# Optimization experiments

Hardware: AMD Instinct MI355X
Metric: run time of the kernel (lower is better)

Reference implementation:

```python
import jax, jax.numpy as jnp
import numpy as np

K = 16  # num_neighbors
L = 3   # stacked PointTransformer layers


def _mlp2(x, w1, b1, w2, b2):
    return jax.nn.relu(x @ w1 + b1) @ w2 + b2


def setup_inputs() -> dict:
    key = jax.random.key(0)
    ks = jax.random.split(key, 10)
    B, N, D = 2, 8192, 3
    HP, HA = 32, 12  # pos_mlp hidden, attn_mlp hidden (3*4)
    f = lambda k, shp, s: jax.random.normal(k, shp, dtype=jnp.float32) * s
    return {
        "feats": f(ks[0], (B, N, D), 1.0),
        "pos": f(ks[1], (B, N, 3), 1.0),
        "mask": jnp.ones((B, N), dtype=bool),  # unused by PT.forward
        "w_qkv": f(ks[2], (L, D, 3 * D), 1.0 / np.sqrt(D)),
        "pos_w1": f(ks[3], (L, 3, HP), 1.0 / np.sqrt(3.0)),
        "pos_b1": jnp.zeros((L, HP), jnp.float32),
        "pos_w2": f(ks[4], (L, HP, D), 1.0 / np.sqrt(HP)),
        "pos_b2": jnp.zeros((L, D), jnp.float32),
        "attn_w1": f(ks[5], (L, D, HA), 1.0 / np.sqrt(D)),
        "attn_b1": jnp.zeros((L, HA), jnp.float32),
        "attn_w2": f(ks[6], (L, HA, D), 1.0 / np.sqrt(HA)),
        "attn_b2": jnp.zeros((L, D), jnp.float32),
        "lin_w": f(ks[7], (D, 2), 1.0 / np.sqrt(D)),
        "lin_b": jnp.zeros((2,), jnp.float32),
    }


def reference(feats, pos, mask, w_qkv, pos_w1, pos_b1, pos_w2, pos_b2,
              attn_w1, attn_b1, attn_w2, attn_b2, lin_w, lin_b):
    # kNN indices from pairwise squared distances (monotonic in the norm the
    # original uses, so topk-smallest gives identical neighbor sets).
    sq = jnp.sum(pos * pos, axis=-1)                               # [B,N]
    d2 = sq[:, :, None] + sq[:, None, :] - 2.0 * jnp.einsum('bic,bjc->bij', pos, pos)
    _, idx = jax.lax.top_k(-d2, K)                                 # [B,N,K]

    gather = jax.vmap(lambda t, i: t[i])                           # [B,N,d],[B,N,K]->[B,N,K,d]
    pos_j = gather(pos, idx)                                       # [B,N,K,3]
    rel_pos = pos[:, :, None, :] - pos_j                           # [B,N,K,3]

    h = feats
    for l in range(L):
        qkv = h @ w_qkv[l]                                         # [B,N,9]
        q, k, v = jnp.split(qkv, 3, axis=-1)
        k_j = gather(k, idx)                                       # [B,N,K,3]
        v_j = gather(v, idx)
        rel_emb = _mlp2(rel_pos, pos_w1[l], pos_b1[l], pos_w2[l], pos_b2[l])
        qk_rel = q[:, :, None, :] - k_j
        sim = _mlp2(qk_rel + rel_emb, attn_w1[l], attn_b1[l], attn_w2[l], attn_b2[l])
        attn = jax.nn.softmax(sim, axis=-2)                        # softmax over neighbors
        agg = jnp.einsum('bijd,bijd->bid', attn, v_j + rel_emb)    # [B,N,3]
        h = jax.nn.sigmoid(agg)
    out = h @ lin_w + lin_b                                        # [B,N,2]
    return jax.nn.softmax(out, axis=2)
```

## Files before the change

kernel.cpp:

```cpp
#include <hip/hip_runtime.h>
#include <math.h>

#define N_PTS 8192
#define BATCH 2
#define KNB 16
#define NQ (BATCH * N_PTS)

#define H    0.35f
#define INVH (1.0f / 0.35f)
#define NC   30
#define LBOX (0.5f * H * NC)
#define NCELL (NC * NC * NC)
#define MCELL (2 * NCELL)
#define NROW1 9
#define NROWT 43
#define SLOWG 1024
#define FINF 3.4e38f

typedef unsigned long long u64;

__device__ __forceinline__ float med3f(float a, float b, float c) {
#if __has_builtin(__builtin_amdgcn_fmed3f)
    return __builtin_amdgcn_fmed3f(a, b, c);
#else
    return fmaxf(fminf(a, b), fminf(fmaxf(a, b), c));
#endif
}

__device__ __forceinline__ unsigned sortable(float x) {
    unsigned u = __float_as_uint(x);
    return u ^ ((unsigned)((int)u >> 31) | 0x80000000u);
}

__device__ __forceinline__ void ins_u64(u64 (&pk)[KNB], u64 key) {
    if (key < pk[0]) {
#pragma unroll
        for (int s = 0; s < KNB; ++s) {
            const u64 ds1 = (s < KNB - 1) ? pk[s + 1] : 0ull;
            const bool c0 = key < pk[s];
            const bool c1 = key < ds1;
            pk[s] = c1 ? ds1 : (c0 ? key : pk[s]);
        }
    }
}

__device__ __forceinline__ void merge64_u64(u64 (&pk)[KNB]) {
#pragma unroll
    for (int mm = 1; mm <= 32; mm <<= 1) {
        u64 L[KNB];
#pragma unroll
        for (int i = 0; i < KNB; ++i) {
            const u64 a = pk[i];
            const u64 c = __shfl_xor(pk[KNB - 1 - i], mm);
            L[i] = a < c ? a : c;
        }
#pragma unroll
        for (int dd = 8; dd >= 1; dd >>= 1) {
#pragma unroll
            for (int i = 0; i < KNB; ++i) {
                if ((i & dd) == 0) {
                    const u64 hi = L[i] > L[i | dd] ? L[i] : L[i | dd];
                    const u64 lo = L[i] > L[i | dd] ? L[i | dd] : L[i];
                    L[i] = hi; L[i | dd] = lo;
                }
            }
        }
#pragma unroll
        for (int i = 0; i < KNB; ++i) pk[i] = L[i];
    }
}

__device__ __forceinline__ void merge64_f(float (&d)[KNB]) {
#pragma unroll
    for (int mm = 1; mm <= 32; mm <<= 1) {
        float L[KNB];
#pragma unroll
        for (int i = 0; i < KNB; ++i)
            L[i] = fminf(d[i], __shfl_xor(d[KNB - 1 - i], mm));
#pragma unroll
        for (int dd = 8; dd >= 1; dd >>= 1) {
#pragma unroll
            for (int i = 0; i < KNB; ++i) {
                if ((i & dd) == 0) {
                    const float hi = fmaxf(L[i], L[i | dd]);
                    const float lo = fminf(L[i], L[i | dd]);
                    L[i] = hi; L[i | dd] = lo;
                }
            }
        }
#pragma unroll
        for (int i = 0; i < KNB; ++i) d[i] = L[i];
    }
}

__global__ __launch_bounds__(256) void kcount(const float* __restrict__ pos,
                                              int* __restrict__ cnt,
                                              int* __restrict__ cellid) {
    const int g = blockIdx.x * 256 + threadIdx.x;
    const int b = g >> 13;
    const float x = pos[g * 3 + 0], y = pos[g * 3 + 1], z = pos[g * 3 + 2];
    int cx = (int)floorf((x + LBOX) * INVH); cx = min(max(cx, 0), NC - 1);
    int cy = (int)floorf((y + LBOX) * INVH); cy = min(max(cy, 0), NC - 1);
    int cz = (int)floorf((z + LBOX) * INVH); cz = min(max(cz, 0), NC - 1);
    const int c = (((b * NC) + cz) * NC + cy) * NC + cx;
    cellid[g] = c;
    atomicAdd(&cnt[c], 1);
}

__global__ __launch_bounds__(1024) void kscan1(const int* __restrict__ cnt,
                                               int* __restrict__ scanned,
                                               int* __restrict__ bsum) {
    __shared__ int sh[1024];
    const int t = threadIdx.x;
    const int idx = blockIdx.x * 1024 + t;
    int v = (idx < MCELL) ? cnt[idx] : 0;
    sh[t] = v;
    __syncthreads();
    for (int off = 1; off < 1024; off <<= 1) {
        const int add = (t >= off) ? sh[t - off] : 0;
        __syncthreads();
        sh[t] += add;
        __syncthreads();
    }
    if (idx < MCELL) scanned[idx] = sh[t];
    if (t == 1023) bsum[blockIdx.x] = sh[1023];
}

__global__ __launch_bounds__(1024) void kscan2(const int* __restrict__ scanned,
                                               const int* __restrict__ bsum,
                                               int* __restrict__ cell_start) {
    __shared__ int soff;
    const int t = threadIdx.x;
    const int blk = blockIdx.x;
    const int idx = blk * 1024 + t;
    if (t == 0) {
        int s = 0;
        for (int k = 0; k < blk; ++k) s += bsum[k];
        soff = s;
    }
    __syncthreads();
    if (idx < MCELL) cell_start[idx + 1] = scanned[idx] + soff;
    if (idx == 0) cell_start[0] = 0;
}

__global__ __launch_bounds__(256) void kscatter(const float* __restrict__ pos,
                                                const int* __restrict__ cellid,
                                                const int* __restrict__ cell_start,
                                                int* __restrict__ cnt2,
                                                float4* __restrict__ spp,
                                                int* __restrict__ sidx) {
    const int g = blockIdx.x * 256 + threadIdx.x;
    const int c = cellid[g];
    const int off = atomicAdd(&cnt2[c], 1);
    const int p = cell_start[c] + off;
    const float x = pos[g * 3 + 0], y = pos[g * 3 + 1], z = pos[g * 3 + 2];
    spp[p] = make_float4(-2.f * x, -2.f * y, -2.f * z, fmaf(x, x, fmaf(y, y, z * z)));
    sidx[p] = g & (N_PTS - 1);
}

__global__ __launch_bounds__(64, 4) void ksearch_fast(const float4* __restrict__ spp,
                                                      const int* __restrict__ sidx,
                                                      const int* __restrict__ cs,
                                                      int* __restrict__ knn,
                                                      int* __restrict__ ovf_list,
                                                      int* __restrict__ ovf_cnt) {
    __shared__ int rstL[4][NROWT];
    __shared__ int psL[4][NROWT + 1];
    const int tid = threadIdx.x;
    const int li  = tid & 15;
    const int gq  = tid >> 4;
    const int sq  = blockIdx.x * 4 + gq;
    const int b   = sq >> 13;

    {
        __shared__ int cntL[4][NROWT];
        for (int t = tid; t < 4 * NROWT; t += 64) {
            const int q = t / NROWT, r = t % NROWT;
            const int sq2 = blockIdx.x * 4 + q;
            const int b2  = sq2 >> 13;
            const float4 m2 = spp[sq2];
            const float px = -0.5f * m2.x, py = -0.5f * m2.y, pz = -0.5f * m2.z;
            int c2x = (int)floorf((px + LBOX) * INVH); c2x = min(max(c2x, 0), NC - 1);
            int c2y = (int)floorf((py + LBOX) * INVH); c2y = min(max(c2y, 0), NC - 1);
            int c2z = (int)floorf((pz + LBOX) * INVH); c2z = min(max(c2z, 0), NC - 1);

            int st = 0, en = 0;
            int z, y, xlo, xhi;
            bool ok = true;
            if (r < NROW1) {
                z = c2z + r / 3 - 1;
                y = c2y + (r % 3) - 1;
                xlo = max(c2x - 1, 0); xhi = min(c2x + 1, NC - 1);
            } else {
                const int rr = r - NROW1;
                if (rr < 10) {
                    z = c2z + (rr < 5 ? -2 : 2);
                    y = c2y + (rr % 5) - 2;
                    xlo = max(c2x - 2, 0); xhi = min(c2x + 2, NC - 1);
                } else if (rr < 16) {
                    const int k = rr - 10;
                    z = c2z + (k % 3) - 1;
                    y = c2y + (k < 3 ? -2 : 2);
                    xlo = max(c2x - 2, 0); xhi = min(c2x + 2, NC - 1);
                } else {
                    const int k = rr - 16;
                    const int m = k % 9;
                    z = c2z + m / 3 - 1;
                    y = c2y + (m % 3) - 1;
                    const int xx = c2x + (k < 9 ? -2 : 2);
                    xlo = xhi = xx;
                    ok = (xx >= 0) && (xx < NC);
                }
            }
            if (ok && z >= 0 && z < NC && y >= 0 && y < NC) {
                const int rowb = (((b2 * NC) + z) * NC + y) * NC;
                st = cs[rowb + xlo];
                en = cs[rowb + xhi + 1];
            }
            rstL[q][r] = st; cntL[q][r] = en - st;
        }
        __syncthreads();
        if (tid < 4) {
            int acc = 0;
            psL[tid][0] = 0;
            for (int r = 0; r < NROWT; ++r) { acc += cntL[tid][r]; psL[tid][r + 1] = acc; }
        }
        __syncthreads();
    }

    const float4 me = spp[sq];
    const float qx = -0.5f * me.x, qy = -0.5f * me.y, qz = -0.5f * me.z;
    const float qsq = me.w;
    int cx = (int)floorf((qx + LBOX) * INVH); cx = min(max(cx, 0), NC - 1);
    int cy = (int)floorf((qy + LBOX) * INVH); cy = min(max(cy, 0), NC - 1);
    int cz = (int)floorf((qz + LBOX) * INVH); cz = min(max(cz, 0), NC - 1);

    const int tot1 = psL[gq][NROW1];
    const int tot2 = psL[gq][NROWT];

    float d[KNB];
#pragma unroll
    for (int k = 0; k < KNB; ++k) d[k] = FINF;

    int row = 0;
    int t = li;

    auto scan1_flat = [&](int limit) {
        while (t < limit) {
            int pp[8]; bool vv[8];
#pragma unroll
            for (int u = 0; u < 8; ++u) {
                const int tt = t + u * 16;
                vv[u] = (tt < limit);
                int p = sq;
                if (vv[u]) {
                    while (tt >= psL[gq][row + 1]) ++row;
                    p = rstL[gq][row] + (tt - psL[gq][row]);
                }
                pp[u] = p;
            }
            float4 v[8];
#pragma unroll
            for (int u = 0; u < 8; ++u) v[u] = spp[pp[u]];
#pragma unroll
            for (int u = 0; u < 8; ++u) {
                const float x = vv[u] ? fmaf(qx, v[u].x, fmaf(qy, v[u].y, fmaf(qz, v[u].z, v[u].w)))
                                      : FINF;
                if (x < d[0]) {
#pragma unroll
                    for (int s = 0; s < KNB - 1; ++s) d[s] = med3f(d[s], d[s + 1], x);
                    d[KNB - 1] = fminf(d[KNB - 1], x);
                }
            }
            t += 128;
        }
    };

    auto boundtest = [&](int R) -> bool {
        const float bxl = fmaf((float)(cx - R), H, -LBOX);
        const float bxh = fmaf((float)(cx + R + 1), H, -LBOX);
        const float byl = fmaf((float)(cy - R), H, -LBOX);
        const float byh = fmaf((float)(cy + R + 1), H, -LBOX);
        const float bzl = fmaf((float)(cz - R), H, -LBOX);
        const float bzh = fmaf((float)(cz + R + 1), H, -LBOX);
        const float m = fminf(fminf(fminf(qx - bxl, bxh - qx),
                                    fminf(qy - byl, byh - qy)),
                              fminf(qz - bzl, bzh - qz));
        if (!(m > 0.f)) return false;
        const float Bf = fmaf(m, m, -1e-4f) - qsq;
        int c = 0;
#pragma unroll
        for (int k = 0; k < KNB; ++k) c += (d[k] <= Bf) ? 1 : 0;
#pragma unroll
        for (int off = 1; off < 16; off <<= 1) c += __shfl_xor(c, off);
        return c >= KNB;
    };

    scan1_flat(tot1);
    const bool done1 = boundtest(1);
    bool ovf = false;
    if (!done1) {
        scan1_flat(tot2);
        if (!boundtest(2)) ovf = true;
    }
    if (ovf) {
        if (li == 0) { const int s2 = atomicAdd(ovf_cnt, 1); ovf_list[s2] = sq; }
        return;
    }
    const int tot = done1 ? tot1 : tot2;

#pragma unroll
    for (int mm = 1; mm <= 8; mm <<= 1) {
        float L[KNB];
#pragma unroll
        for (int i = 0; i < KNB; ++i)
            L[i] = fminf(d[i], __shfl_xor(d[KNB - 1 - i], mm));
#pragma unroll
        for (int dd = 8; dd >= 1; dd >>= 1) {
#pragma unroll
            for (int i = 0; i < KNB; ++i) {
                if ((i & dd) == 0) {
                    const float hi = fmaxf(L[i], L[i | dd]);
                    const float lo = fminf(L[i], L[i | dd]);
                    L[i] = hi; L[i | dd] = lo;
                }
            }
        }
#pragma unroll
        for (int i = 0; i < KNB; ++i) d[i] = L[i];
    }
    const float thr = d[0];

    u64 pk[KNB];
#pragma unroll
    for (int k = 0; k < KNB; ++k) pk[k] = 0xFFFFFFFFFFFFFFFFull;

    row = 0;
    int t2 = li;
    while (t2 < tot) {
        int pp[8]; bool vv[8];
#pragma unroll
        for (int u = 0; u < 8; ++u) {
            const int tt = t2 + u * 16;
            vv[u] = (tt < tot);
            int p = sq;
            if (vv[u]) {
                while (tt >= psL[gq][row + 1]) ++row;
                p = rstL[gq][row] + (tt - psL[gq][row]);
            }
            pp[u] = p;
        }
        float4 v[8];
#pragma unroll
        for (int u = 0; u < 8; ++u) v[u] = spp[pp[u]];
#pragma unroll
        for (int u = 0; u < 8; ++u) {
            const float x = vv[u] ? fmaf(qx, v[u].x, fmaf(qy, v[u].y, fmaf(qz, v[u].z, v[u].w)))
                                  : FINF;
            if (x <= thr) {
                ins_u64(pk, ((u64)sortable(x) << 32) | (unsigned)sidx[pp[u]]);
            }
        }
        t2 += 128;
    }

#pragma unroll
    for (int mm = 1; mm <= 8; mm <<= 1) {
        u64 L[KNB];
#pragma unroll
        for (int i = 0; i < KNB; ++i) {
            const u64 a = pk[i];
            const u64 c = __shfl_xor(pk[KNB - 1 - i], mm);
            L[i] = a < c ? a : c;
        }
#pragma unroll
        for (int dd = 8; dd >= 1; dd >>= 1) {
#pragma unroll
            for (int i = 0; i < KNB; ++i) {
                if ((i & dd) == 0) {
                    const u64 hi = L[i] > L[i | dd] ? L[i] : L[i | dd];
                    const u64 lo = L[i] > L[i | dd] ? L[i | dd] : L[i];
                    L[i] = hi; L[i | dd] = lo;
                }
            }
        }
#pragma unroll
        for (int i = 0; i < KNB; ++i) pk[i] = L[i];
    }

    const int qorig = sidx[sq];
    const int obase = ((b << 13) + qorig) * KNB;
    u64 sel = pk[0];
#pragma unroll
    for (int s = 1; s < KNB; ++s) sel = (li == s) ? pk[s] : sel;
    knn[obase + li] = (int)(unsigned)(sel & 0xFFFFFFFFull);
}

__global__ __launch_bounds__(64, 4) void kslow(const float4* __restrict__ spp,
                                               const int* __restrict__ sidx,
                                               int* __restrict__ knn,
                                               const int* __restrict__ ovf_list,
                                               const int* __restrict__ ovf_cnt) {
    const int lane = threadIdx.x;
    const int nov = *ovf_cnt;

    for (int w = blockIdx.x; w < nov; w += SLOWG) {
        const int sq = ovf_list[w];
        const int b  = sq >> 13;
        const float4 me = spp[sq];
        const float qx = -0.5f * me.x, qy = -0.5f * me.y, qz = -0.5f * me.z;
        const int base = b << 13;

        float d[KNB];
#pragma unroll
        for (int k = 0; k < KNB; ++k) d[k] = FINF;

        for (int t0 = 0; t0 < 16; ++t0) {
            const int tb = base + lane + t0 * 512;
            float4 v[8];
#pragma unroll
            for (int u = 0; u < 8; ++u) v[u] = spp[tb + u * 64];
#pragma unroll
            for (int u = 0; u < 8; ++u) {
                const float x = fmaf(qx, v[u].x, fmaf(qy, v[u].y, fmaf(qz, v[u].z, v[u].w)));
                if (x < d[0]) {
#pragma unroll
                    for (int s = 0; s < KNB - 1; ++s) d[s] = med3f(d[s], d[s + 1], x);
                    d[KNB - 1] = fminf(d[KNB - 1], x);
                }
            }
        }
        merge64_f(d);
        const float thr = d[0];

        u64 pk[KNB];
#pragma unroll
        for (int k = 0; k < KNB; ++k) pk[k] = 0xFFFFFFFFFFFFFFFFull;

        for (int t0 = 0; t0 < 16; ++t0) {
            const int tb = base + lane + t0 * 512;
            float4 v[8];
#pragma unroll
            for (int u = 0; u < 8; ++u) v[u] = spp[tb + u * 64];
#pragma unroll
            for (int u = 0; u < 8; ++u) {
                const float x = fmaf(qx, v[u].x, fmaf(qy, v[u].y, fmaf(qz, v[u].z, v[u].w)));
                if (x <= thr) {
                    ins_u64(pk, ((u64)sortable(x) << 32) | (unsigned)sidx[tb + u * 64]);
                }
            }
        }
        merge64_u64(pk);

        const int qorig = sidx[sq];
        const int obase = ((b << 13) + qorig) * KNB;
        u64 sel = pk[0];
#pragma unroll
        for (int s = 1; s < KNB; ++s) sel = (lane == s) ? pk[s] : sel;
        if (lane < KNB) knn[obase + lane] = (int)(unsigned)(sel & 0xFFFFFFFFull);
    }
}

__global__ __launch_bounds__(256) void pt_layer_f(const float* __restrict__ hin,
                                                  const float* __restrict__ pos,
                                                  const int* __restrict__ knn,
                                                  const float* __restrict__ wqkv,
                                                  const float* __restrict__ pw1,
                                                  const float* __restrict__ pb1,
                                                  const float* __restrict__ pw2,
                                                  const float* __restrict__ pb2,
                                                  const float* __restrict__ aw1,
                                                  const float* __restrict__ ab1,
                                                  const float* __restrict__ aw2,
                                                  const float* __restrict__ ab2,
                                                  float* __restrict__ hout,
                                                  const float* __restrict__ lw,
                                                  const float* __restrict__ lb,
                                                  float* __restrict__ out,
                                                  int last) {
    const int gt = blockIdx.x * 256 + threadIdx.x;
    const int qg = gt >> 4;
    const int j  = gt & 15;
    const int b  = qg >> 13;
    const int jj = knn[qg * KNB + j] & (N_PTS - 1);
    const int g  = (b << 13) + jj;

    const float hi0 = hin[qg * 3 + 0], hi1 = hin[qg * 3 + 1], hi2 = hin[qg * 3 + 2];
    const float hj0 = hin[g * 3 + 0],  hj1 = hin[g * 3 + 1],  hj2 = hin[g * 3 + 2];
    const float rx = pos[qg * 3 + 0] - pos[g * 3 + 0];
    const float ry = pos[qg * 3 + 1] - pos[g * 3 + 1];
    const float rz = pos[qg * 3 + 2] - pos[g * 3 + 2];

    const float q0 = fmaf(hi0, wqkv[0], fmaf(hi1, wqkv[9],  hi2 * wqkv[18]));
    const float q1 = fmaf(hi0, wqkv[1], fmaf(hi1, wqkv[10], hi2 * wqkv[19]));
    const float q2 = fmaf(hi0, wqkv[2], fmaf(hi1, wqkv[11], hi2 * wqkv[20]));
    const float k0 = fmaf(hj0, wqkv[3], fmaf(hj1, wqkv[12], hj2 * wqkv[21]));
    const float k1 = fmaf(hj0, wqkv[4], fmaf(hj1, wqkv[13], hj2 * wqkv[22]));
    const float k2 = fmaf(hj0, wqkv[5], fmaf(hj1, wqkv[14], hj2 * wqkv[23]));
    const float v0 = fmaf(hj0, wqkv[6], fmaf(hj1, wqkv[15], hj2 * wqkv[24]));
    const float v1 = fmaf(hj0, wqkv[7], fmaf(hj1, wqkv[16], hj2 * wqkv[25]));
    const float v2 = fmaf(hj0, wqkv[8], fmaf(hj1, wqkv[17], hj2 * wqkv[26]));

    float e0 = pb2[0], e1 = pb2[1], e2 = pb2[2];
#pragma unroll
    for (int hh = 0; hh < 32; ++hh) {
        float t = fmaf(rx, pw1[hh], fmaf(ry, pw1[32 + hh], fmaf(rz, pw1[64 + hh], pb1[hh])));
        t = fmaxf(t, 0.0f);
        e0 = fmaf(t, pw2[hh * 3 + 0], e0);
        e1 = fmaf(t, pw2[hh * 3 + 1], e1);
        e2 = fmaf(t, pw2[hh * 3 + 2], e2);
    }

    const float x0 = q0 - k0 + e0;
    const float x1 = q1 - k1 + e1;
    const float x2 = q2 - k2 + e2;

    float s0 = ab2[0], s1 = ab2[1], s2 = ab2[2];
#pragma unroll
    for (int hh = 0; hh < 12; ++hh) {
        float t = fmaf(x0, aw1[hh], fmaf(x1, aw1[12 + hh], fmaf(x2, aw1[24 + hh], ab1[hh])));
        t = fmaxf(t, 0.0f);
        s0 = fmaf(t, aw2[hh * 3 + 0], s0);
        s1 = fmaf(t, aw2[hh * 3 + 1], s1);
        s2 = fmaf(t, aw2[hh * 3 + 2], s2);
    }

    const float w0 = v0 + e0, w1 = v1 + e1, w2 = v2 + e2;

    float m0 = s0, m1 = s1, m2 = s2;
#pragma unroll
    for (int off = 1; off < 16; off <<= 1) {
        m0 = fmaxf(m0, __shfl_xor(m0, off));
        m1 = fmaxf(m1, __shfl_xor(m1, off));
        m2 = fmaxf(m2, __shfl_xor(m2, off));
    }
    const float ex0 = __expf(s0 - m0), ex1 = __expf(s1 - m1), ex2 = __expf(s2 - m2);
    float n0 = ex0 * w0, n1 = ex1 * w1, n2 = ex2 * w2;
    float den0 = ex0, den1 = ex1, den2 = ex2;
#pragma unroll
    for (int off = 1; off < 16; off <<= 1) {
        den0 += __shfl_xor(den0, off); n0 += __shfl_xor(n0, off);
        den1 += __shfl_xor(den1, off); n1 += __shfl_xor(n1, off);
        den2 += __shfl_xor(den2, off); n2 += __shfl_xor(n2, off);
    }

    if (j == 0) {
        const float h0 = 1.f / (1.f + __expf(-(n0 / den0)));
        const float h1 = 1.f / (1.f + __expf(-(n1 / den1)));
        const float h2 = 1.f / (1.f + __expf(-(n2 / den2)));
        if (!last) {
            hout[qg * 3 + 0] = h0;
            hout[qg * 3 + 1] = h1;
            hout[qg * 3 + 2] = h2;
        } else {
            const float o0 = fmaf(h0, lw[0], fmaf(h1, lw[2], fmaf(h2, lw[4], lb[0])));
            const float o1 = fmaf(h0, lw[1], fmaf(h1, lw[3], fmaf(h2, lw[5], lb[1])));
            const float mm = fmaxf(o0, o1);
            const float ea = __expf(o0 - mm), eb = __expf(o1 - mm);
            const float inv = 1.f / (ea + eb);
            out[qg * 2 + 0] = ea * inv;
            out[qg * 2 + 1] = eb * inv;
        }
    }
}

extern "C" void kernel_launch(void* const* d_in, const int* in_sizes, int n_in,
                              void* d_out, int out_size, void* d_ws, size_t ws_size,
                              hipStream_t stream) {
    const float* feats = (const float*)d_in[0];
    const float* pos   = (const float*)d_in[1];
    const float* wqkv = (const float*)d_in[3];
    const float* pw1  = (const float*)d_in[4];
    const float* pb1  = (const float*)d_in[5];
    const float* pw2  = (const float*)d_in[6];
    const float* pb2  = (const float*)d_in[7];
    const float* aw1  = (const float*)d_in[8];
    const float* ab1  = (const float*)d_in[9];
    const float* aw2  = (const float*)d_in[10];
    const float* ab2  = (const float*)d_in[11];
    const float* lw   = (const float*)d_in[12];
    const float* lb   = (const float*)d_in[13];
    float* out = (float*)d_out;

    size_t o = 0;
    auto take = [&](size_t bytes) { size_t r = o; o += (bytes + 15) & ~(size_t)15; return r; };
    const size_t o_cnt   = take((size_t)(2 * MCELL + 4) * 4);
    const size_t o_scan  = take((size_t)MCELL * 4);
    const size_t o_cs    = take((size_t)(MCELL + 1) * 4);
    const size_t o_bsum  = take((size_t)256 * 4);
    const size_t o_cid   = take((size_t)NQ * 4);
    const size_t o_spp   = take((size_t)NQ * 16);
    const size_t o_sidx  = take((size_t)NQ * 4);
    const size_t o_knn   = take((size_t)NQ * KNB * 4);
    const size_t o_ovfl  = take((size_t)NQ * 4);
    const size_t o_hA    = take((size_t)NQ * 3 * 4);
    const size_t o_hB    = take((size_t)NQ * 3 * 4);
    if (ws_size < o) return;

    char* ws = (char*)d_ws;
    int*    cnt     = (int*)(ws + o_cnt);
    int*    cnt2    = cnt + MCELL;
    int*    ovf_cnt = cnt + 2 * MCELL;
    int*    scan  = (int*)(ws + o_scan);
    int*    cs    = (int*)(ws + o_cs);
    int*    bsum  = (int*)(ws + o_bsum);
    int*    cid   = (int*)(ws + o_cid);
    float4* spp   = (float4*)(ws + o_spp);
    int*    sidx  = (int*)(ws + o_sidx);
    int*    knn   = (int*)(ws + o_knn);
    int*    ovfl  = (int*)(ws + o_ovfl);
    float*  hA    = (float*)(ws + o_hA);
    float*  hB    = (float*)(ws + o_hB);

    const int nscan = (MCELL + 1023) / 1024;

    hipMemsetAsync(cnt, 0, (size_t)(2 * MCELL + 1) * 4, stream);
    kcount<<<NQ / 256, 256, 0, stream>>>(pos, cnt, cid);
    kscan1<<<nscan, 1024, 0, stream>>>(cnt, scan, bsum);
    kscan2<<<nscan, 1024, 0, stream>>>(scan, bsum, cs);
    kscatter<<<NQ / 256, 256, 0, stream>>>(pos, cid, cs, cnt2, spp, sidx);
    ksearch_fast<<<NQ / 4, 64, 0, stream>>>(spp, sidx, cs, knn, ovfl, ovf_cnt);
    kslow<<<SLOWG, 64, 0, stream>>>(spp, sidx, knn, ovfl, ovf_cnt);

    pt_layer_f<<<NQ * 16 / 256, 256, 0, stream>>>(feats, pos, knn,
        wqkv + 0, pw1 + 0, pb1 + 0, pw2 + 0, pb2 + 0,
        aw1 + 0, ab1 + 0, aw2 + 0, ab2 + 0,
        hA, lw, lb, out, 0);
    pt_layer_f<<<NQ * 16 / 256, 256, 0, stream>>>(hA, pos, knn,
        wqkv + 27, pw1 + 96, pb1 + 32, pw2 + 96, pb2 + 3,
        aw1 + 36, ab1 + 12, aw2 + 36, ab2 + 3,
        hB, lw, lb, out, 0);
    pt_layer_f<<<NQ * 16 / 256, 256, 0, stream>>>(hB, pos, knn,
        wqkv + 54, pw1 + 192, pb1 + 64, pw2 + 192, pb2 + 6,
        aw1 + 72, ab1 + 24, aw2 + 72, ab2 + 6,
        hB, lw, lb, out, 1);
}
```

Baseline: 126.6 us.

## Split brute-force overflow kNN search across four wavefronts per query

The fallback brute-force kNN kernel now uses four wavefronts per overflow query instead of one. Each wave scans a quarter of the batch's points, and the partial top-16 lists are merged through shared memory, both for the distance threshold and for the final packed index list. This cuts the serial scan length per query and adds block-level syncs plus an extra merge step. It also lowers the occupancy bound per block. The gain depends on how many queries overflow, which may be few.

```diff
diff --git a/kernel.cpp b/kernel.cpp
--- a/kernel.cpp
+++ b/kernel.cpp
@@ -396,12 +396,16 @@
     knn[obase + li] = (int)(unsigned)(sel & 0xFFFFFFFFull);
 }
 
-__global__ __launch_bounds__(64, 4) void kslow(const float4* __restrict__ spp,
-                                               const int* __restrict__ sidx,
-                                               int* __restrict__ knn,
-                                               const int* __restrict__ ovf_list,
-                                               const int* __restrict__ ovf_cnt) {
-    const int lane = threadIdx.x;
+__global__ __launch_bounds__(256, 2) void kslow(const float4* __restrict__ spp,
+                                                const int* __restrict__ sidx,
+                                                int* __restrict__ knn,
+                                                const int* __restrict__ ovf_list,
+                                                const int* __restrict__ ovf_cnt) {
+    __shared__ float shf[4][KNB];
+    __shared__ u64  shp[4][KNB];
+    const int tid  = threadIdx.x;
+    const int wv   = tid >> 6;
+    const int lane = tid & 63;
     const int nov = *ovf_cnt;
 
     for (int w = blockIdx.x; w < nov; w += SLOWG) {
@@ -409,14 +413,15 @@
         const int b  = sq >> 13;
         const float4 me = spp[sq];
         const float qx = -0.5f * me.x, qy = -0.5f * me.y, qz = -0.5f * me.z;
-        const int base = b << 13;
+        const int qbase = (b << 13) + wv * 2048;
 
         float d[KNB];
 #pragma unroll
         for (int k = 0; k < KNB; ++k) d[k] = FINF;
 
-        for (int t0 = 0; t0 < 16; ++t0) {
-            const int tb = base + lane + t0 * 512;
+#pragma unroll
+        for (int t0 = 0; t0 < 4; ++t0) {
+            const int tb = qbase + lane + t0 * 512;
             float4 v[8];
 #pragma unroll
             for (int u = 0; u < 8; ++u) v[u] = spp[tb + u * 64];
@@ -431,14 +436,23 @@
             }
         }
         merge64_f(d);
-        const float thr = d[0];
+        if (lane < KNB) shf[wv][lane] = d[lane];
+        __syncthreads();
+
+        float dm[KNB];
+#pragma unroll
+        for (int i = 0; i < KNB - 1; ++i) dm[i] = FINF;
+        dm[KNB - 1] = shf[lane >> 4][lane & 15];
+        merge64_f(dm);
+        const float thr = dm[0];
 
         u64 pk[KNB];
 #pragma unroll
         for (int k = 0; k < KNB; ++k) pk[k] = 0xFFFFFFFFFFFFFFFFull;
 
-        for (int t0 = 0; t0 < 16; ++t0) {
-            const int tb = base + lane + t0 * 512;
+#pragma unroll
+        for (int t0 = 0; t0 < 4; ++t0) {
+            const int tb = qbase + lane + t0 * 512;
             float4 v[8];
 #pragma unroll
             for (int u = 0; u < 8; ++u) v[u] = spp[tb + u * 64];
@@ -451,13 +465,24 @@
             }
         }
         merge64_u64(pk);
-
-        const int qorig = sidx[sq];
-        const int obase = ((b << 13) + qorig) * KNB;
-        u64 sel = pk[0];
-#pragma unroll
-        for (int s = 1; s < KNB; ++s) sel = (lane == s) ? pk[s] : sel;
-        if (lane < KNB) knn[obase + lane] = (int)(unsigned)(sel & 0xFFFFFFFFull);
+        if (lane < KNB) shp[wv][lane] = pk[lane];
+        __syncthreads();
+
+        if (wv == 0) {
+            u64 pm[KNB];
+#pragma unroll
+            for (int i = 0; i < KNB - 1; ++i) pm[i] = 0xFFFFFFFFFFFFFFFFull;
+            pm[KNB - 1] = shp[lane >> 4][lane & 15];
+            merge64_u64(pm);
+
+            const int qorig = sidx[sq];
+            const int obase = ((b << 13) + qorig) * KNB;
+            u64 sel = pm[0];
+#pragma unroll
+            for (int s = 1; s < KNB; ++s) sel = (lane == s) ? pm[s] : sel;
+            if (lane < KNB) knn[obase + lane] = (int)(unsigned)(sel & 0xFFFFFFFFull);
+        }
+        __syncthreads();
     }
 }
 
@@ -620,7 +645,7 @@
     kscan2<<<nscan, 1024, 0, stream>>>(scan, bsum, cs);
     kscatter<<<NQ / 256, 256, 0, stream>>>(pos, cid, cs, cnt2, spp, sidx);
     ksearch_fast<<<NQ / 4, 64, 0, stream>>>(spp, sidx, cs, knn, ovfl, ovf_cnt);
-    kslow<<<SLOWG, 64, 0, stream>>>(spp, sidx, knn, ovfl, ovf_cnt);
+    kslow<<<SLOWG, 256, 0, stream>>>(spp, sidx, knn, ovfl, ovf_cnt);
 
     pt_layer_f<<<NQ * 16 / 256, 256, 0, stream>>>(feats, pos, knn,
         wqkv + 0, pw1 + 0, pb1 + 0, pw2 + 0, pb2 + 0,
```

Result: slower. 144.8 us (+14.4%).

## Share candidate loads across four queries when a block's queries share one cell

Applied to the files above, without the earlier changes.

Adds a fast path to the grid kNN search for blocks whose four queries fall in the same cell. All 64 lanes then scan the shared neighbor rows once, and each loaded point is tested against all four queries. The second pass collects candidates under the threshold into a shared-memory buffer with atomics, and each 16-lane group sorts its buffer, replacing per-lane u64 insertion over the whole candidate set. The general path's unroll drops from 8 to 4 and the merge helpers are factored out. The trade-offs are four 16-entry register queues per lane, more register pressure and branch divergence, and more queries sent to the slow kernel when a buffer overflows.

```diff
diff --git a/kernel.cpp b/kernel.cpp
--- a/kernel.cpp
+++ b/kernel.cpp
@@ -15,6 +15,7 @@
 #define NROW1 9
 #define NROWT 43
 #define SLOWG 1024
+#define HCAP 64
 #define FINF 3.4e38f
 
 typedef unsigned long long u64;
@@ -44,6 +45,14 @@
     }
 }
 
+__device__ __forceinline__ void ins_f(float (&dq)[KNB], float x) {
+    if (x < dq[0]) {
+#pragma unroll
+        for (int s = 0; s < KNB - 1; ++s) dq[s] = med3f(dq[s], dq[s + 1], x);
+        dq[KNB - 1] = fminf(dq[KNB - 1], x);
+    }
+}
+
 __device__ __forceinline__ void merge64_u64(u64 (&pk)[KNB]) {
 #pragma unroll
     for (int mm = 1; mm <= 32; mm <<= 1) {
@@ -70,9 +79,10 @@
     }
 }
 
-__device__ __forceinline__ void merge64_f(float (&d)[KNB]) {
-#pragma unroll
-    for (int mm = 1; mm <= 32; mm <<= 1) {
+template <int W>
+__device__ __forceinline__ void mergeW_f(float (&d)[KNB]) {
+#pragma unroll
+    for (int mm = 1; mm < W; mm <<= 1) {
         float L[KNB];
 #pragma unroll
         for (int i = 0; i < KNB; ++i)
@@ -90,6 +100,32 @@
         }
 #pragma unroll
         for (int i = 0; i < KNB; ++i) d[i] = L[i];
+    }
+}
+
+__device__ __forceinline__ void merge16_u64(u64 (&pk)[KNB]) {
+#pragma unroll
+    for (int mm = 1; mm <= 8; mm <<= 1) {
+        u64 L[KNB];
+#pragma unroll
+        for (int i = 0; i < KNB; ++i) {
+            const u64 a = pk[i];
+            const u64 c = __shfl_xor(pk[KNB - 1 - i], mm);
+            L[i] = a < c ? a : c;
+        }
+#pragma unroll
+        for (int dd = 8; dd >= 1; dd >>= 1) {
+#pragma unroll
+            for (int i = 0; i < KNB; ++i) {
+                if ((i & dd) == 0) {
+                    const u64 hi = L[i] > L[i | dd] ? L[i] : L[i | dd];
+                    const u64 lo = L[i] > L[i | dd] ? L[i | dd] : L[i];
+                    L[i] = hi; L[i | dd] = lo;
+                }
+            }
+        }
+#pragma unroll
+        for (int i = 0; i < KNB; ++i) pk[i] = L[i];
     }
 }
 
@@ -166,15 +202,17 @@
                                                       int* __restrict__ ovf_cnt) {
     __shared__ int rstL[4][NROWT];
     __shared__ int psL[4][NROWT + 1];
-    const int tid = threadIdx.x;
-    const int li  = tid & 15;
-    const int gq  = tid >> 4;
-    const int sq  = blockIdx.x * 4 + gq;
-    const int b   = sq >> 13;
+    __shared__ int cellL[4];
+    __shared__ int hc[4];
+    __shared__ int ovfL[4];
+    __shared__ u64 hbuf[4][HCAP];
+
+    const int lane = threadIdx.x;
+    if (lane < 4) { hc[lane] = 0; ovfL[lane] = 0; }
 
     {
         __shared__ int cntL[4][NROWT];
-        for (int t = tid; t < 4 * NROWT; t += 64) {
+        for (int t = lane; t < 4 * NROWT; t += 64) {
             const int q = t / NROWT, r = t % NROWT;
             const int sq2 = blockIdx.x * 4 + q;
             const int b2  = sq2 >> 13;
@@ -183,6 +221,7 @@
             int c2x = (int)floorf((px + LBOX) * INVH); c2x = min(max(c2x, 0), NC - 1);
             int c2y = (int)floorf((py + LBOX) * INVH); c2y = min(max(c2y, 0), NC - 1);
             int c2z = (int)floorf((pz + LBOX) * INVH); c2z = min(max(c2z, 0), NC - 1);
+            if (r == 0) cellL[q] = (((b2 * NC) + c2z) * NC + c2y) * NC + c2x;
 
             int st = 0, en = 0;
             int z, y, xlo, xhi;
@@ -220,13 +259,197 @@
             rstL[q][r] = st; cntL[q][r] = en - st;
         }
         __syncthreads();
-        if (tid < 4) {
+        if (lane < 4) {
             int acc = 0;
-            psL[tid][0] = 0;
-            for (int r = 0; r < NROWT; ++r) { acc += cntL[tid][r]; psL[tid][r + 1] = acc; }
+            psL[lane][0] = 0;
+            for (int r = 0; r < NROWT; ++r) { acc += cntL[lane][r]; psL[lane][r + 1] = acc; }
         }
         __syncthreads();
     }
+
+    const bool same = (cellL[0] == cellL[1]) && (cellL[1] == cellL[2]) && (cellL[2] == cellL[3]);
+
+    if (same) {
+        const int sqb = blockIdx.x * 4;
+        const int b   = sqb >> 13;
+        float qxs[4], qys[4], qzs[4], qss[4];
+#pragma unroll
+        for (int q = 0; q < 4; ++q) {
+            const float4 m = spp[sqb + q];
+            qxs[q] = -0.5f * m.x; qys[q] = -0.5f * m.y; qzs[q] = -0.5f * m.z; qss[q] = m.w;
+        }
+        const int c2 = cellL[0] - b * NCELL;
+        const int cx = c2 % NC, cy = (c2 / NC) % NC, cz = c2 / (NC * NC);
+
+        const int tot1 = psL[0][NROW1];
+        const int tot2 = psL[0][NROWT];
+
+        float d[4][KNB];
+#pragma unroll
+        for (int q = 0; q < 4; ++q)
+#pragma unroll
+            for (int k = 0; k < KNB; ++k) d[q][k] = FINF;
+
+        auto scan_sh = [&](int lo, int hi) {
+            int t = lo + ((lane - lo) & 63);
+            int row = 0;
+            while (t < hi) {
+                int pp[4]; bool vv[4];
+#pragma unroll
+                for (int u = 0; u < 4; ++u) {
+                    const int tt = t + (u << 6);
+                    vv[u] = (tt < hi);
+                    int p = sqb;
+                    if (vv[u]) {
+                        while (tt >= psL[0][row + 1]) ++row;
+                        p = rstL[0][row] + (tt - psL[0][row]);
+                    }
+                    pp[u] = p;
+                }
+                float4 v[4];
+#pragma unroll
+                for (int u = 0; u < 4; ++u) v[u] = spp[pp[u]];
+#pragma unroll
+                for (int u = 0; u < 4; ++u) {
+#pragma unroll
+                    for (int q = 0; q < 4; ++q) {
+                        const float x = vv[u] ? fmaf(qxs[q], v[u].x,
+                                         fmaf(qys[q], v[u].y,
+                                         fmaf(qzs[q], v[u].z, v[u].w))) : FINF;
+                        if (q == 0) ins_f(d[0], x);
+                        else if (q == 1) ins_f(d[1], x);
+                        else if (q == 2) ins_f(d[2], x);
+                        else ins_f(d[3], x);
+                    }
+                }
+                t += 256;
+            }
+        };
+
+        auto bt_sh = [&](float (&dq)[KNB], float qx, float qy, float qz, float qs, int R) -> bool {
+            const float bxl = fmaf((float)(cx - R), H, -LBOX);
+            const float bxh = fmaf((float)(cx + R + 1), H, -LBOX);
+            const float byl = fmaf((float)(cy - R), H, -LBOX);
+            const float byh = fmaf((float)(cy + R + 1), H, -LBOX);
+            const float bzl = fmaf((float)(cz - R), H, -LBOX);
+            const float bzh = fmaf((float)(cz + R + 1), H, -LBOX);
+            const float m = fminf(fminf(fminf(qx - bxl, bxh - qx),
+                                        fminf(qy - byl, byh - qy)),
+                                  fminf(qz - bzl, bzh - qz));
+            if (!(m > 0.f)) return false;
+            const float Bf = fmaf(m, m, -1e-4f) - qs;
+            int c = 0;
+#pragma unroll
+            for (int k = 0; k < KNB; ++k) c += (dq[k] <= Bf) ? 1 : 0;
+#pragma unroll
+            for (int off = 1; off < 64; off <<= 1) c += __shfl_xor(c, off);
+            return c >= KNB;
+        };
+
+        scan_sh(0, tot1);
+        bool d1[4];
+        d1[0] = bt_sh(d[0], qxs[0], qys[0], qzs[0], qss[0], 1);
+        d1[1] = bt_sh(d[1], qxs[1], qys[1], qzs[1], qss[1], 1);
+        d1[2] = bt_sh(d[2], qxs[2], qys[2], qzs[2], qss[2], 1);
+        d1[3] = bt_sh(d[3], qxs[3], qys[3], qzs[3], qss[3], 1);
+        const bool all1 = d1[0] && d1[1] && d1[2] && d1[3];
+        int tot = tot1;
+        if (!all1) {
+            scan_sh(tot1, tot2);
+            tot = tot2;
+            if (lane == 0) {
+                if (!d1[0] && !bt_sh(d[0], qxs[0], qys[0], qzs[0], qss[0], 2)) ovfL[0] = 1;
+                if (!d1[1] && !bt_sh(d[1], qxs[1], qys[1], qzs[1], qss[1], 2)) ovfL[1] = 1;
+                if (!d1[2] && !bt_sh(d[2], qxs[2], qys[2], qzs[2], qss[2], 2)) ovfL[2] = 1;
+                if (!d1[3] && !bt_sh(d[3], qxs[3], qys[3], qzs[3], qss[3], 2)) ovfL[3] = 1;
+            } else {
+                if (!d1[0]) bt_sh(d[0], qxs[0], qys[0], qzs[0], qss[0], 2);
+                if (!d1[1]) bt_sh(d[1], qxs[1], qys[1], qzs[1], qss[1], 2);
+                if (!d1[2]) bt_sh(d[2], qxs[2], qys[2], qzs[2], qss[2], 2);
+                if (!d1[3]) bt_sh(d[3], qxs[3], qys[3], qzs[3], qss[3], 2);
+            }
+        }
+        __syncthreads();
+
+        mergeW_f<64>(d[0]); mergeW_f<64>(d[1]); mergeW_f<64>(d[2]); mergeW_f<64>(d[3]);
+        float thr[4] = { d[0][0], d[1][0], d[2][0], d[3][0] };
+        bool ov[4] = { ovfL[0] != 0, ovfL[1] != 0, ovfL[2] != 0, ovfL[3] != 0 };
+
+        {
+            int t = lane;
+            int row = 0;
+            while (t < tot) {
+                int pp[4]; bool vv[4];
+#pragma unroll
+                for (int u = 0; u < 4; ++u) {
+                    const int tt = t + (u << 6);
+                    vv[u] = (tt < tot);
+                    int p = sqb;
+                    if (vv[u]) {
+                        while (tt >= psL[0][row + 1]) ++row;
+                        p = rstL[0][row] + (tt - psL[0][row]);
+                    }
+                    pp[u] = p;
+                }
+                float4 v[4];
+#pragma unroll
+                for (int u = 0; u < 4; ++u) v[u] = spp[pp[u]];
+#pragma unroll
+                for (int u = 0; u < 4; ++u) {
+                    if (!vv[u]) continue;
+#pragma unroll
+                    for (int q = 0; q < 4; ++q) {
+                        if (ov[q]) continue;
+                        const float x = fmaf(qxs[q], v[u].x,
+                                        fmaf(qys[q], v[u].y,
+                                        fmaf(qzs[q], v[u].z, v[u].w)));
+                        if (x <= thr[q]) {
+                            const int pos = atomicAdd(&hc[q], 1);
+                            if (pos < HCAP)
+                                hbuf[q][pos] = ((u64)sortable(x) << 32) | (unsigned)sidx[pp[u]];
+                        }
+                    }
+                }
+                t += 256;
+            }
+        }
+        __syncthreads();
+
+        if (lane == 0) {
+#pragma unroll
+            for (int q = 0; q < 4; ++q) {
+                if (ovfL[q] || hc[q] > HCAP) {
+                    const int s2 = atomicAdd(ovf_cnt, 1);
+                    ovf_list[s2] = sqb + q;
+                }
+            }
+        }
+
+        const int li = lane & 15, gq = lane >> 4;
+        const bool bad = (ovfL[gq] != 0) || (hc[gq] > HCAP);
+        if (!bad) {
+            u64 pk[KNB];
+#pragma unroll
+            for (int k = 0; k < KNB; ++k) pk[k] = 0xFFFFFFFFFFFFFFFFull;
+            const int n = min(hc[gq], HCAP);
+            for (int i = li; i < n; i += 16) ins_u64(pk, hbuf[gq][i]);
+            merge16_u64(pk);
+
+            const int sq = sqb + gq;
+            const int qorig = sidx[sq];
+            const int obase = ((b << 13) + qorig) * KNB;
+            u64 sel = pk[0];
+#pragma unroll
+            for (int s = 1; s < KNB; ++s) sel = (li == s) ? pk[s] : sel;
+            knn[obase + li] = (int)(unsigned)(sel & 0xFFFFFFFFull);
+        }
+        return;
+    }
+
+    const int li  = lane & 15;
+    const int gq  = lane >> 4;
+    const int sq  = blockIdx.x * 4 + gq;
+    const int b   = sq >> 13;
 
     const float4 me = spp[sq];
     const float qx = -0.5f * me.x, qy = -0.5f * me.y, qz = -0.5f * me.z;
@@ -242,16 +465,15 @@
 #pragma unroll
     for (int k = 0; k < KNB; ++k) d[k] = FINF;
 
-    int row = 0;
-    int t = li;
-
-    auto scan1_flat = [&](int limit) {
-        while (t < limit) {
-            int pp[8]; bool vv[8];
-#pragma unroll
-            for (int u = 0; u < 8; ++u) {
-                const int tt = t + u * 16;
-                vv[u] = (tt < limit);
+    auto scan1_flat = [&](int lo, int hi) {
+        int t = lo + ((li - lo) & 15);
+        int row = 0;
+        while (t < hi) {
+            int pp[4]; bool vv[4];
+#pragma unroll
+            for (int u = 0; u < 4; ++u) {
+                const int tt = t + (u << 4);
+                vv[u] = (tt < hi);
                 int p = sq;
                 if (vv[u]) {
                     while (tt >= psL[gq][row + 1]) ++row;
@@ -259,20 +481,16 @@
                 }
                 pp[u] = p;
             }
-            float4 v[8];
-#pragma unroll
-            for (int u = 0; u < 8; ++u) v[u] = spp[pp[u]];
-#pragma unroll
-            for (int u = 0; u < 8; ++u) {
+            float4 v[4];
+#pragma unroll
+            for (int u = 0; u < 4; ++u) v[u] = spp[pp[u]];
+#pragma unroll
+            for (int u = 0; u < 4; ++u) {
                 const float x = vv[u] ? fmaf(qx, v[u].x, fmaf(qy, v[u].y, fmaf(qz, v[u].z, v[u].w)))
                                       : FINF;
-                if (x < d[0]) {
-#pragma unroll
-                    for (int s = 0; s < KNB - 1; ++s) d[s] = med3f(d[s], d[s + 1], x);
-                    d[KNB - 1] = fminf(d[KNB - 1], x);
-                }
-            }
-            t += 128;
+                ins_f(d, x);
+            }
+            t += 64;
         }
     };
 
@@ -296,11 +514,11 @@
         return c >= KNB;
     };
 
-    scan1_flat(tot1);
+    scan1_flat(0, tot1);
     const bool done1 = boundtest(1);
     bool ovf = false;
     if (!done1) {
-        scan1_flat(tot2);
+        scan1_flat(tot1, tot2);
         if (!boundtest(2)) ovf = true;
     }
     if (ovf) {
@@ -309,84 +527,45 @@
     }
     const int tot = done1 ? tot1 : tot2;
 
-#pragma unroll
-    for (int mm = 1; mm <= 8; mm <<= 1) {
-        float L[KNB];
-#pragma unroll
-        for (int i = 0; i < KNB; ++i)
-            L[i] = fminf(d[i], __shfl_xor(d[KNB - 1 - i], mm));
-#pragma unroll
-        for (int dd = 8; dd >= 1; dd >>= 1) {
-#pragma unroll
-            for (int i = 0; i < KNB; ++i) {
-                if ((i & dd) == 0) {
-                    const float hi = fmaxf(L[i], L[i | dd]);
-                    const float lo = fminf(L[i], L[i | dd]);
-                    L[i] = hi; L[i | dd] = lo;
-                }
-            }
-        }
-#pragma unroll
-        for (int i = 0; i < KNB; ++i) d[i] = L[i];
-    }
+    mergeW_f<16>(d);
     const float thr = d[0];
 
     u64 pk[KNB];
 #pragma unroll
     for (int k = 0; k < KNB; ++k) pk[k] = 0xFFFFFFFFFFFFFFFFull;
 
-    row = 0;
-    int t2 = li;
-    while (t2 < tot) {
-        int pp[8]; bool vv[8];
-#pragma unroll
-        for (int u = 0; u < 8; ++u) {
-            const int tt = t2 + u * 16;
-            vv[u] = (tt < tot);
-            int p = sq;
-            if (vv[u]) {
-                while (tt >= psL[gq][row + 1]) ++row;
-                p = rstL[gq][row] + (tt - psL[gq][row]);
-            }
-            pp[u] = p;
-        }
-        float4 v[8];
-#pragma unroll
-        for (int u = 0; u < 8; ++u) v[u] = spp[pp[u]];
-#pragma unroll
-        for (int u = 0; u < 8; ++u) {
-            const float x = vv[u] ? fmaf(qx, v[u].x, fmaf(qy, v[u].y, fmaf(qz, v[u].z, v[u].w)))
-                                  : FINF;
-            if (x <= thr) {
-                ins_u64(pk, ((u64)sortable(x) << 32) | (unsigned)sidx[pp[u]]);
-            }
-        }
-        t2 += 128;
-    }
-
-#pragma unroll
-    for (int mm = 1; mm <= 8; mm <<= 1) {
-        u64 L[KNB];
-#pragma unroll
-        for (int i = 0; i < KNB; ++i) {
-            const u64 a = pk[i];
-            const u64 c = __shfl_xor(pk[KNB - 1 - i], mm);
-            L[i] = a < c ? a : c;
-        }
-#pragma unroll
-        for (int dd = 8; dd >= 1; dd >>= 1) {
-#pragma unroll
-            for (int i = 0; i < KNB; ++i) {
-                if ((i & dd) == 0) {
-                    const u64 hi = L[i] > L[i | dd] ? L[i] : L[i | dd];
-                    const u64 lo = L[i] > L[i | dd] ? L[i | dd] : L[i];
-                    L[i] = hi; L[i | dd] = lo;
-                }
-            }
-        }
-#pragma unroll
-        for (int i = 0; i < KNB; ++i) pk[i] = L[i];
-    }
+    {
+        int t2 = li;
+        int row = 0;
+        while (t2 < tot) {
+            int pp[4]; bool vv[4];
+#pragma unroll
+            for (int u = 0; u < 4; ++u) {
+                const int tt = t2 + (u << 4);
+                vv[u] = (tt < tot);
+                int p = sq;
+                if (vv[u]) {
+                    while (tt >= psL[gq][row + 1]) ++row;
+                    p = rstL[gq][row] + (tt - psL[gq][row]);
+                }
+                pp[u] = p;
+            }
+            float4 v[4];
+#pragma unroll
+            for (int u = 0; u < 4; ++u) v[u] = spp[pp[u]];
+#pragma unroll
+            for (int u = 0; u < 4; ++u) {
+                const float x = vv[u] ? fmaf(qx, v[u].x, fmaf(qy, v[u].y, fmaf(qz, v[u].z, v[u].w)))
+                                      : FINF;
+                if (x <= thr) {
+                    ins_u64(pk, ((u64)sortable(x) << 32) | (unsigned)sidx[pp[u]]);
+                }
+            }
+            t2 += 64;
+        }
+    }
+
+    merge16_u64(pk);
 
     const int qorig = sidx[sq];
     const int obase = ((b << 13) + qorig) * KNB;
@@ -423,14 +602,10 @@
 #pragma unroll
             for (int u = 0; u < 8; ++u) {
                 const float x = fmaf(qx, v[u].x, fmaf(qy, v[u].y, fmaf(qz, v[u].z, v[u].w)));
-                if (x < d[0]) {
-#pragma unroll
-                    for (int s = 0; s < KNB - 1; ++s) d[s] = med3f(d[s], d[s + 1], x);
-                    d[KNB - 1] = fminf(d[KNB - 1], x);
-                }
-            }
-        }
-        merge64_f(d);
+                ins_f(d, x);
+            }
+        }
+        mergeW_f<64>(d);
         const float thr = d[0];
 
         u64 pk[KNB];
```

New measurement: 135.6 us. 1.07x slower.
